# Kernel optimization log

Measured on AMD Instinct MI355X. Metric: run time of the kernel, lower is better.

## Reference

```python
import jax, jax.numpy as jnp
import numpy as np
from jax import lax

B, TIN, N, M, O, LM, TDEC = 64, 128, 256, 1024, 512, 2048, 64
LN_EPS = 1e-5


def setup_inputs() -> dict:
    key = jax.random.key(0)
    ks = jax.random.split(key, 32)
    s = 0.02
    p = lambda k, shape: (jax.random.normal(k, shape, jnp.float32) * s)
    z = lambda n: jnp.zeros((n,), jnp.float32)
    return {
        "X": jax.random.normal(ks[0], (B, TIN, N), jnp.float32),
        "Y0": jax.random.uniform(ks[1], (B, 1, O), jnp.float32),
        # encoder GRU, 2 layers (PyTorch layout: W_ih [3m,in], W_hh [3m,m])
        "enc_Wih0": p(ks[2], (3 * M, N)), "enc_Whh0": p(ks[3], (3 * M, M)),
        "enc_bih0": z(3 * M), "enc_bhh0": z(3 * M),
        "enc_Wih1": p(ks[4], (3 * M, M)), "enc_Whh1": p(ks[5], (3 * M, M)),
        "enc_bih1": z(3 * M), "enc_bhh1": z(3 * M),
        # decoder GRU, 2 layers (layer0 input dim = O)
        "dec_Wih0": p(ks[6], (3 * M, O)), "dec_Whh0": p(ks[7], (3 * M, M)),
        "dec_bih0": z(3 * M), "dec_bhh0": z(3 * M),
        "dec_Wih1": p(ks[8], (3 * M, M)), "dec_Whh1": p(ks[9], (3 * M, M)),
        "dec_bih1": z(3 * M), "dec_bhh1": z(3 * M),
        # decoder head
        "fc1_w": p(ks[10], (LM, M)), "fc1_b": z(LM),
        "ln_g": jnp.ones((LM,), jnp.float32), "ln_b": z(LM),
        "fc2_w": p(ks[11], (O, LM)), "fc2_b": z(O),
    }


def _gru_step(h, x, Wih, Whh, bih, bhh):
    # PyTorch GRU cell: gates ordered (r, z, n)
    gi = x @ Wih.T + bih          # [B, 3m]
    gh = h @ Whh.T + bhh          # [B, 3m]
    i_r, i_z, i_n = jnp.split(gi, 3, axis=-1)
    h_r, h_z, h_n = jnp.split(gh, 3, axis=-1)
    r = jax.nn.sigmoid(i_r + h_r)
    zg = jax.nn.sigmoid(i_z + h_z)
    n = jnp.tanh(i_n + r * h_n)
    return (1.0 - zg) * n + zg * h


def reference(X, Y0,
              enc_Wih0, enc_Whh0, enc_bih0, enc_bhh0,
              enc_Wih1, enc_Whh1, enc_bih1, enc_bhh1,
              dec_Wih0, dec_Whh0, dec_bih0, dec_bhh0,
              dec_Wih1, dec_Whh1, dec_bih1, dec_bhh1,
              fc1_w, fc1_b, ln_g, ln_b, fc2_w, fc2_b):
    batch = X.shape[0]
    # ---- encoder: 2-layer GRU over time ----
    seq = jnp.swapaxes(X, 0, 1)  # [T, B, n]
    enc_layers = [(enc_Wih0, enc_Whh0, enc_bih0, enc_bhh0),
                  (enc_Wih1, enc_Whh1, enc_bih1, enc_bhh1)]
    h_final = []
    for (Wih, Whh, bih, bhh) in enc_layers:
        def f(h, x, Wih=Wih, Whh=Whh, bih=bih, bhh=bhh):
            hn = _gru_step(h, x, Wih, Whh, bih, bhh)
            return hn, hn
        hT, seq = lax.scan(f, jnp.zeros((batch, M), X.dtype), seq)
        h_final.append(hT)

    dec0 = (dec_Wih0, dec_Whh0, dec_bih0, dec_bhh0)
    dec1 = (dec_Wih1, dec_Whh1, dec_bih1, dec_bhh1)
    y_init = Y0[:, 0, :]  # [B, o]

    def step(carry, _):
        h0, h1, y = carry
        h0n = _gru_step(h0, y, *dec0)
        h1n = _gru_step(h1, h0n, *dec1)
        z = h1n @ fc1_w.T + fc1_b                      # [B, l_m]
        mu = jnp.mean(z, axis=-1, keepdims=True)
        var = jnp.var(z, axis=-1, keepdims=True)
        z = (z - mu) * lax.rsqrt(var + LN_EPS) * ln_g + ln_b
        z = jax.nn.gelu(z, approximate=False)
        out = z @ fc2_w.T + fc2_b                      # [B, o]
        yn = jax.nn.softmax(out, axis=-1)
        return (h0n, h1n, yn), out

    _, outs = lax.scan(step, (h_final[0], h_final[1], y_init), None, length=TDEC)
    return jnp.swapaxes(outs, 0, 1)  # [B, TDEC, o]
```

## Files before the change

kernel.cpp:

```cpp
#include <hip/hip_runtime.h>
#include <math.h>

#define B 64
#define TIN 128
#define N_IN 256
#define M 1024
#define O_DIM 512
#define LM 2048
#define TDEC 64
#define M3 3072
#define CH 8

typedef short bf16x8 __attribute__((ext_vector_type(8)));
typedef float floatx4 __attribute__((ext_vector_type(4)));

__device__ __forceinline__ unsigned short f2bf(float f) {
    unsigned int u = __float_as_uint(f);
    u += 0x7FFFu + ((u >> 16) & 1u);
    return (unsigned short)(u >> 16);
}
__device__ __forceinline__ float sigm(float x) { return 1.f / (1.f + expf(-x)); }

__global__ __launch_bounds__(256) void cast_bf(const float* __restrict__ in,
                                               short* __restrict__ out, int n) {
    int i = blockIdx.x * 256 + threadIdx.x;
    if (i < n) out[i] = (short)f2bf(in[i]);
}

__global__ __launch_bounds__(256) void transpose_X_bf(const float* __restrict__ X,
                                                      short* __restrict__ Xt) {
    int idx = blockIdx.x * 256 + threadIdx.x;
    int n = idx & (N_IN - 1);
    int b = (idx >> 8) & (B - 1);
    int t = idx >> 14;
    Xt[idx] = (short)f2bf(X[(b * TIN + t) * N_IN + n]);
}

__global__ __launch_bounds__(256) void mfma_gemm_bias(
    const short* __restrict__ A, int lda,
    const short* __restrict__ W, int ldw,
    const float* __restrict__ bias,
    float* __restrict__ C, int ldc, int K) {
    int wave = threadIdx.x >> 6;
    int lane = threadIdx.x & 63;
    int r0 = blockIdx.y * 64 + wave * 16;
    int c0 = blockIdx.x * 16;
    int lrow = lane & 15;
    int ko8 = (lane >> 4) * 8;
    const short* ap = A + (size_t)(r0 + lrow) * lda + ko8;
    const short* wp = W + (size_t)(c0 + lrow) * ldw + ko8;
    floatx4 acc = {0.f, 0.f, 0.f, 0.f};
    #pragma unroll 4
    for (int k = 0; k < K; k += 32) {
        bf16x8 a = *(const bf16x8*)(ap + k);
        bf16x8 b = *(const bf16x8*)(wp + k);
        acc = __builtin_amdgcn_mfma_f32_16x16x32_bf16(a, b, acc, 0, 0, 0);
    }
    int col = c0 + lrow;
    float bv = bias[col];
    int rbase = r0 + (lane >> 4) * 4;
    #pragma unroll
    for (int i = 0; i < 4; i++)
        C[(size_t)(rbase + i) * ldc + col] = acc[i] + bv;
}

__global__ __launch_bounds__(256) void mfma_gemm_bias_ks(
    const short* __restrict__ A, int lda,
    const short* __restrict__ W, int ldw,
    const float* __restrict__ bias,
    float* __restrict__ C, int ldc, int K) {
    __shared__ float lds[4][64][4];
    int wave = threadIdx.x >> 6;
    int lane = threadIdx.x & 63;
    int r0 = blockIdx.y * 16;
    int c0 = blockIdx.x * 16;
    int Kq = K >> 2;
    int lrow = lane & 15;
    int ko8 = (lane >> 4) * 8;
    const short* ap = A + (size_t)(r0 + lrow) * lda + wave * Kq + ko8;
    const short* wp = W + (size_t)(c0 + lrow) * ldw + wave * Kq + ko8;
    floatx4 acc = {0.f, 0.f, 0.f, 0.f};
    #pragma unroll 4
    for (int k = 0; k < Kq; k += 32) {
        bf16x8 a = *(const bf16x8*)(ap + k);
        bf16x8 b = *(const bf16x8*)(wp + k);
        acc = __builtin_amdgcn_mfma_f32_16x16x32_bf16(a, b, acc, 0, 0, 0);
    }
    #pragma unroll
    for (int i = 0; i < 4; i++) lds[wave][lane][i] = acc[i];
    __syncthreads();
    int row = threadIdx.x >> 4, col = threadIdx.x & 15;
    int sl = (row >> 2) * 16 + col, rg = row & 3;
    float s = lds[0][sl][rg] + lds[1][sl][rg] + lds[2][sl][rg] + lds[3][sl][rg];
    C[(size_t)(r0 + row) * ldc + (c0 + col)] = s + bias[c0 + col];
}

__global__ __launch_bounds__(256) void gru_step_enc(
    const short* __restrict__ h_in_bf, const short* __restrict__ Whh,
    const float* __restrict__ gi, const float* __restrict__ bhh,
    float* __restrict__ h_f, short* __restrict__ h_out_bf,
    short* __restrict__ seq_out_bf) {
    __shared__ float lr[4][64][4], lz[4][64][4], lnn[4][64][4];
    int wave = threadIdx.x >> 6;
    int lane = threadIdx.x & 63;
    int m0 = blockIdx.x * 16;
    int r0 = blockIdx.y * 16;
    int lrow = lane & 15;
    int ko8 = (lane >> 4) * 8;
    const int Kq = M >> 2;
    const short* ap = h_in_bf + (size_t)(r0 + lrow) * M + wave * Kq + ko8;
    const short* wr = Whh + (size_t)(m0 + lrow) * M + wave * Kq + ko8;
    const short* wz = wr + (size_t)M * M;
    const short* wn = wr + (size_t)2 * M * M;
    floatx4 ar = {0.f, 0.f, 0.f, 0.f};
    floatx4 az = {0.f, 0.f, 0.f, 0.f};
    floatx4 ahn = {0.f, 0.f, 0.f, 0.f};
    #pragma unroll
    for (int k = 0; k < Kq; k += 32) {
        bf16x8 a = *(const bf16x8*)(ap + k);
        ar  = __builtin_amdgcn_mfma_f32_16x16x32_bf16(a, *(const bf16x8*)(wr + k), ar, 0, 0, 0);
        az  = __builtin_amdgcn_mfma_f32_16x16x32_bf16(a, *(const bf16x8*)(wz + k), az, 0, 0, 0);
        ahn = __builtin_amdgcn_mfma_f32_16x16x32_bf16(a, *(const bf16x8*)(wn + k), ahn, 0, 0, 0);
    }
    #pragma unroll
    for (int i = 0; i < 4; i++) {
        lr[wave][lane][i] = ar[i];
        lz[wave][lane][i] = az[i];
        lnn[wave][lane][i] = ahn[i];
    }
    __syncthreads();
    int row = threadIdx.x >> 4, col = threadIdx.x & 15;
    int sl = (row >> 2) * 16 + col, rg = row & 3;
    float sr = lr[0][sl][rg] + lr[1][sl][rg] + lr[2][sl][rg] + lr[3][sl][rg];
    float sz = lz[0][sl][rg] + lz[1][sl][rg] + lz[2][sl][rg] + lz[3][sl][rg];
    float sn = lnn[0][sl][rg] + lnn[1][sl][rg] + lnn[2][sl][rg] + lnn[3][sl][rg];
    int b = r0 + row, m = m0 + col;
    const float* gir = gi + (size_t)b * M3;
    float r = sigm(gir[m] + sr + bhh[m]);
    float z = sigm(gir[M + m] + sz + bhh[M + m]);
    float n = tanhf(gir[2 * M + m] + r * (sn + bhh[2 * M + m]));
    size_t hi = (size_t)b * M + m;
    float hv = (1.f - z) * n + z * h_f[hi];
    h_f[hi] = hv;
    short hb = (short)f2bf(hv);
    h_out_bf[hi] = hb;
    if (seq_out_bf) seq_out_bf[hi] = hb;
}

__global__ __launch_bounds__(256) void gru_step_dec(
    const short* __restrict__ x_bf, int Kx,
    const short* __restrict__ Wih,
    const short* __restrict__ h_in_bf, const short* __restrict__ Whh,
    const float* __restrict__ bih, const float* __restrict__ bhh,
    float* __restrict__ h_f, short* __restrict__ h_out_bf) {
    __shared__ float lr[4][64][4], lz[4][64][4], li[4][64][4], lh[4][64][4];
    int wave = threadIdx.x >> 6;
    int lane = threadIdx.x & 63;
    int m0 = blockIdx.x * 16;
    int r0 = blockIdx.y * 16;
    int lrow = lane & 15;
    int ko8 = (lane >> 4) * 8;
    floatx4 ar = {0.f, 0.f, 0.f, 0.f};
    floatx4 az = {0.f, 0.f, 0.f, 0.f};
    floatx4 ain = {0.f, 0.f, 0.f, 0.f};
    floatx4 ahn = {0.f, 0.f, 0.f, 0.f};
    {
        int Kq = Kx >> 2;
        const short* ap = x_bf + (size_t)(r0 + lrow) * Kx + wave * Kq + ko8;
        const short* wr = Wih + (size_t)(m0 + lrow) * Kx + wave * Kq + ko8;
        const short* wz = wr + (size_t)M * Kx;
        const short* wn = wr + (size_t)2 * M * Kx;
        #pragma unroll
        for (int k = 0; k < Kq; k += 32) {
            bf16x8 a = *(const bf16x8*)(ap + k);
            ar  = __builtin_amdgcn_mfma_f32_16x16x32_bf16(a, *(const bf16x8*)(wr + k), ar, 0, 0, 0);
            az  = __builtin_amdgcn_mfma_f32_16x16x32_bf16(a, *(const bf16x8*)(wz + k), az, 0, 0, 0);
            ain = __builtin_amdgcn_mfma_f32_16x16x32_bf16(a, *(const bf16x8*)(wn + k), ain, 0, 0, 0);
        }
    }
    {
        const int Kq = M >> 2;
        const short* ap = h_in_bf + (size_t)(r0 + lrow) * M + wave * Kq + ko8;
        const short* wr = Whh + (size_t)(m0 + lrow) * M + wave * Kq + ko8;
        const short* wz = wr + (size_t)M * M;
        const short* wn = wr + (size_t)2 * M * M;
        #pragma unroll
        for (int k = 0; k < Kq; k += 32) {
            bf16x8 a = *(const bf16x8*)(ap + k);
            ar  = __builtin_amdgcn_mfma_f32_16x16x32_bf16(a, *(const bf16x8*)(wr + k), ar, 0, 0, 0);
            az  = __builtin_amdgcn_mfma_f32_16x16x32_bf16(a, *(const bf16x8*)(wz + k), az, 0, 0, 0);
            ahn = __builtin_amdgcn_mfma_f32_16x16x32_bf16(a, *(const bf16x8*)(wn + k), ahn, 0, 0, 0);
        }
    }
    #pragma unroll
    for (int i = 0; i < 4; i++) {
        lr[wave][lane][i] = ar[i];
        lz[wave][lane][i] = az[i];
        li[wave][lane][i] = ain[i];
        lh[wave][lane][i] = ahn[i];
    }
    __syncthreads();
    int row = threadIdx.x >> 4, col = threadIdx.x & 15;
    int sl = (row >> 2) * 16 + col, rg = row & 3;
    float sr = lr[0][sl][rg] + lr[1][sl][rg] + lr[2][sl][rg] + lr[3][sl][rg];
    float sz = lz[0][sl][rg] + lz[1][sl][rg] + lz[2][sl][rg] + lz[3][sl][rg];
    float si = li[0][sl][rg] + li[1][sl][rg] + li[2][sl][rg] + li[3][sl][rg];
    float sh = lh[0][sl][rg] + lh[1][sl][rg] + lh[2][sl][rg] + lh[3][sl][rg];
    int b = r0 + row, m = m0 + col;
    float r = sigm(sr + bih[m] + bhh[m]);
    float z = sigm(sz + bih[M + m] + bhh[M + m]);
    float n = tanhf(si + bih[2 * M + m] + r * (sh + bhh[2 * M + m]));
    size_t hi = (size_t)b * M + m;
    float hv = (1.f - z) * n + z * h_f[hi];
    h_f[hi] = hv;
    h_out_bf[hi] = (short)f2bf(hv);
}

__global__ __launch_bounds__(256) void ln_gelu(const float* __restrict__ z,
                                               const float* __restrict__ g,
                                               const float* __restrict__ bt,
                                               short* __restrict__ zo) {
    __shared__ float red1[4], red2[4];
    int b = blockIdx.x, t = threadIdx.x;
    const float* row = z + (size_t)b * LM;
    float s = 0.f, ss = 0.f;
    for (int i = t; i < LM; i += 256) { float v = row[i]; s += v; ss += v * v; }
    #pragma unroll
    for (int off = 32; off > 0; off >>= 1) {
        s += __shfl_down(s, off, 64);
        ss += __shfl_down(ss, off, 64);
    }
    if ((t & 63) == 0) { red1[t >> 6] = s; red2[t >> 6] = ss; }
    __syncthreads();
    float S = red1[0] + red1[1] + red1[2] + red1[3];
    float SS = red2[0] + red2[1] + red2[2] + red2[3];
    float mu = S * (1.f / LM);
    float var = SS * (1.f / LM) - mu * mu;
    float inv = rsqrtf(var + 1e-5f);
    for (int i = t; i < LM; i += 256) {
        float v = (row[i] - mu) * inv * g[i] + bt[i];
        float gv = 0.5f * v * (1.f + erff(v * 0.70710678118654752f));
        zo[(size_t)b * LM + i] = (short)f2bf(gv);
    }
}

__global__ __launch_bounds__(256) void softmax_row(const float* __restrict__ logits,
                                                   int ldl, short* __restrict__ y) {
    __shared__ float redm[4], reds[4];
    int b = blockIdx.x, t = threadIdx.x;
    const float* row = logits + (size_t)b * ldl;
    float v0 = row[t], v1 = row[t + 256];
    float mx = fmaxf(v0, v1);
    #pragma unroll
    for (int off = 32; off > 0; off >>= 1) mx = fmaxf(mx, __shfl_down(mx, off, 64));
    if ((t & 63) == 0) redm[t >> 6] = mx;
    __syncthreads();
    mx = fmaxf(fmaxf(redm[0], redm[1]), fmaxf(redm[2], redm[3]));
    float e0 = expf(v0 - mx), e1 = expf(v1 - mx);
    float s = e0 + e1;
    #pragma unroll
    for (int off = 32; off > 0; off >>= 1) s += __shfl_down(s, off, 64);
    if ((t & 63) == 0) reds[t >> 6] = s;
    __syncthreads();
    s = reds[0] + reds[1] + reds[2] + reds[3];
    float inv = 1.f / s;
    y[b * O_DIM + t] = (short)f2bf(e0 * inv);
    y[b * O_DIM + t + 256] = (short)f2bf(e1 * inv);
}

extern "C" void kernel_launch(void* const* d_in, const int* in_sizes, int n_in,
                              void* d_out, int out_size, void* d_ws, size_t ws_size,
                              hipStream_t stream) {
    const float* X        = (const float*)d_in[0];
    const float* Y0       = (const float*)d_in[1];
    const float* enc_Wih0 = (const float*)d_in[2];
    const float* enc_Whh0 = (const float*)d_in[3];
    const float* enc_bih0 = (const float*)d_in[4];
    const float* enc_bhh0 = (const float*)d_in[5];
    const float* enc_Wih1 = (const float*)d_in[6];
    const float* enc_Whh1 = (const float*)d_in[7];
    const float* enc_bih1 = (const float*)d_in[8];
    const float* enc_bhh1 = (const float*)d_in[9];
    const float* dec_Wih0 = (const float*)d_in[10];
    const float* dec_Whh0 = (const float*)d_in[11];
    const float* dec_bih0 = (const float*)d_in[12];
    const float* dec_bhh0 = (const float*)d_in[13];
    const float* dec_Wih1 = (const float*)d_in[14];
    const float* dec_Whh1 = (const float*)d_in[15];
    const float* dec_bih1 = (const float*)d_in[16];
    const float* dec_bhh1 = (const float*)d_in[17];
    const float* fc1_w    = (const float*)d_in[18];
    const float* fc1_b    = (const float*)d_in[19];
    const float* ln_g     = (const float*)d_in[20];
    const float* ln_b     = (const float*)d_in[21];
    const float* fc2_w    = (const float*)d_in[22];
    const float* fc2_b    = (const float*)d_in[23];
    float* out = (float*)d_out;

    char* p = (char*)d_ws;
    auto carve = [&](size_t bytes) {
        void* r = p;
        p += (bytes + 255) & ~(size_t)255;
        return r;
    };
    short* Xt    = (short*)carve((size_t)TIN * B * N_IN * 2);
    short* seqA  = (short*)carve((size_t)TIN * B * M * 2);
    float* gi_ch = (float*)carve((size_t)CH * B * M3 * 4);
    short* we_ih0 = (short*)carve((size_t)M3 * N_IN * 2);
    short* we_hh0 = (short*)carve((size_t)M3 * M * 2);
    short* we_ih1 = (short*)carve((size_t)M3 * M * 2);
    short* we_hh1 = (short*)carve((size_t)M3 * M * 2);
    short* wd_ih0 = (short*)carve((size_t)M3 * O_DIM * 2);
    short* wd_hh0 = (short*)carve((size_t)M3 * M * 2);
    short* wd_ih1 = (short*)carve((size_t)M3 * M * 2);
    short* wd_hh1 = (short*)carve((size_t)M3 * M * 2);
    short* wfc1   = (short*)carve((size_t)LM * M * 2);
    short* wfc2   = (short*)carve((size_t)O_DIM * LM * 2);
    float* h0f = (float*)carve((size_t)B * M * 4);
    float* h1f = (float*)carve((size_t)B * M * 4);
    short* h0b = (short*)carve((size_t)2 * B * M * 2);
    short* h1b = (short*)carve((size_t)2 * B * M * 2);
    short* yb  = (short*)carve((size_t)B * O_DIM * 2);
    float* zb  = (float*)carve((size_t)B * LM * 4);
    short* zbb = (short*)carve((size_t)B * LM * 2);

    auto cast = [&](const float* src, short* dst, int n) {
        cast_bf<<<(n + 255) / 256, 256, 0, stream>>>(src, dst, n);
    };
    cast(enc_Wih0, we_ih0, M3 * N_IN);
    cast(enc_Whh0, we_hh0, M3 * M);
    cast(enc_Wih1, we_ih1, M3 * M);
    cast(enc_Whh1, we_hh1, M3 * M);
    cast(dec_Wih0, wd_ih0, M3 * O_DIM);
    cast(dec_Whh0, wd_hh0, M3 * M);
    cast(dec_Wih1, wd_ih1, M3 * M);
    cast(dec_Whh1, wd_hh1, M3 * M);
    cast(fc1_w, wfc1, LM * M);
    cast(fc2_w, wfc2, O_DIM * LM);
    cast(Y0, yb, B * O_DIM);
    transpose_X_bf<<<(TIN * B * N_IN) / 256, 256, 0, stream>>>(X, Xt);

    hipMemsetAsync(h0f, 0, (size_t)B * M * 4, stream);
    hipMemsetAsync(h1f, 0, (size_t)B * M * 4, stream);
    hipMemsetAsync(h0b, 0, (size_t)B * M * 2, stream);
    hipMemsetAsync(h1b, 0, (size_t)B * M * 2, stream);

    dim3 gruGrid(M / 16, B / 16);

    for (int layer = 0; layer < 2; layer++) {
        const short* Wih = layer ? we_ih1 : we_ih0;
        const short* Whh = layer ? we_hh1 : we_hh0;
        const float* bih = layer ? enc_bih1 : enc_bih0;
        const float* bhh = layer ? enc_bhh1 : enc_bhh0;
        const short* inseq = layer ? seqA : Xt;
        const int Kin = layer ? M : N_IN;
        float* hf = layer ? h1f : h0f;
        short* hb = layer ? h1b : h0b;
        for (int c = 0; c < TIN / CH; c++) {
            mfma_gemm_bias<<<dim3(M3 / 16, CH * B / 64), 256, 0, stream>>>(
                inseq + (size_t)c * CH * B * Kin, Kin, Wih, Kin, bih,
                gi_ch, M3, Kin);
            for (int tt = 0; tt < CH; tt++) {
                int t = c * CH + tt;
                int pin = t & 1, pout = pin ^ 1;
                short* so = (layer == 0) ? (seqA + (size_t)t * B * M) : nullptr;
                gru_step_enc<<<gruGrid, 256, 0, stream>>>(
                    hb + (size_t)pin * B * M, Whh,
                    gi_ch + (size_t)tt * B * M3, bhh,
                    hf, hb + (size_t)pout * B * M, so);
            }
        }
    }

    for (int t = 0; t < TDEC; t++) {
        int pin = t & 1, pout = pin ^ 1;
        gru_step_dec<<<gruGrid, 256, 0, stream>>>(
            yb, O_DIM, wd_ih0,
            h0b + (size_t)pin * B * M, wd_hh0,
            dec_bih0, dec_bhh0, h0f, h0b + (size_t)pout * B * M);
        gru_step_dec<<<gruGrid, 256, 0, stream>>>(
            h0b + (size_t)pout * B * M, M, wd_ih1,
            h1b + (size_t)pin * B * M, wd_hh1,
            dec_bih1, dec_bhh1, h1f, h1b + (size_t)pout * B * M);
        mfma_gemm_bias_ks<<<dim3(LM / 16, B / 16), 256, 0, stream>>>(
            h1b + (size_t)pout * B * M, M, wfc1, M, fc1_b, zb, LM, M);
        ln_gelu<<<B, 256, 0, stream>>>(zb, ln_g, ln_b, zbb);
        mfma_gemm_bias_ks<<<dim3(O_DIM / 16, B / 16), 256, 0, stream>>>(
            zbb, LM, wfc2, LM, fc2_b, out + (size_t)t * O_DIM, TDEC * O_DIM, LM);
        softmax_row<<<B, 256, 0, stream>>>(out + (size_t)t * O_DIM,
                                           TDEC * O_DIM, yb);
    }
}
```

Before: 5.534 ms.

## Wavefront-fuse encoder GRU layers and fold softmax and LayerNorm into neighbouring GEMMs

```diff
diff --git a/kernel.cpp b/kernel.cpp
--- a/kernel.cpp
+++ b/kernel.cpp
@@ -64,11 +64,260 @@
         C[(size_t)(rbase + i) * ldc + col] = acc[i] + bv;
 }
 
-__global__ __launch_bounds__(256) void mfma_gemm_bias_ks(
+__device__ __forceinline__ void gru_dec_core(
+    const short* x_bf, int Kx,
+    const short* Wih,
+    const short* h_in_bf, const short* Whh,
+    const float* bih, const float* bhh,
+    float* h_f, short* h_out_bf,
+    float (*lr)[64][4], float (*lz)[64][4],
+    float (*li)[64][4], float (*lh)[64][4]) {
+    int wave = threadIdx.x >> 6;
+    int lane = threadIdx.x & 63;
+    int m0 = blockIdx.x * 16;
+    int r0 = blockIdx.y * 16;
+    int lrow = lane & 15;
+    int ko8 = (lane >> 4) * 8;
+    floatx4 ar = {0.f, 0.f, 0.f, 0.f};
+    floatx4 az = {0.f, 0.f, 0.f, 0.f};
+    floatx4 ain = {0.f, 0.f, 0.f, 0.f};
+    floatx4 ahn = {0.f, 0.f, 0.f, 0.f};
+    {
+        int Kq = Kx >> 2;
+        const short* ap = x_bf + (size_t)(r0 + lrow) * Kx + wave * Kq + ko8;
+        const short* wr = Wih + (size_t)(m0 + lrow) * Kx + wave * Kq + ko8;
+        const short* wz = wr + (size_t)M * Kx;
+        const short* wn = wr + (size_t)2 * M * Kx;
+        #pragma unroll
+        for (int k = 0; k < Kq; k += 32) {
+            bf16x8 a = *(const bf16x8*)(ap + k);
+            ar  = __builtin_amdgcn_mfma_f32_16x16x32_bf16(a, *(const bf16x8*)(wr + k), ar, 0, 0, 0);
+            az  = __builtin_amdgcn_mfma_f32_16x16x32_bf16(a, *(const bf16x8*)(wz + k), az, 0, 0, 0);
+            ain = __builtin_amdgcn_mfma_f32_16x16x32_bf16(a, *(const bf16x8*)(wn + k), ain, 0, 0, 0);
+        }
+    }
+    {
+        const int Kq = M >> 2;
+        const short* ap = h_in_bf + (size_t)(r0 + lrow) * M + wave * Kq + ko8;
+        const short* wr = Whh + (size_t)(m0 + lrow) * M + wave * Kq + ko8;
+        const short* wz = wr + (size_t)M * M;
+        const short* wn = wr + (size_t)2 * M * M;
+        #pragma unroll
+        for (int k = 0; k < Kq; k += 32) {
+            bf16x8 a = *(const bf16x8*)(ap + k);
+            ar  = __builtin_amdgcn_mfma_f32_16x16x32_bf16(a, *(const bf16x8*)(wr + k), ar, 0, 0, 0);
+            az  = __builtin_amdgcn_mfma_f32_16x16x32_bf16(a, *(const bf16x8*)(wz + k), az, 0, 0, 0);
+            ahn = __builtin_amdgcn_mfma_f32_16x16x32_bf16(a, *(const bf16x8*)(wn + k), ahn, 0, 0, 0);
+        }
+    }
+    #pragma unroll
+    for (int i = 0; i < 4; i++) {
+        lr[wave][lane][i] = ar[i];
+        lz[wave][lane][i] = az[i];
+        li[wave][lane][i] = ain[i];
+        lh[wave][lane][i] = ahn[i];
+    }
+    __syncthreads();
+    int row = threadIdx.x >> 4, col = threadIdx.x & 15;
+    int sl = (row >> 2) * 16 + col, rg = row & 3;
+    float sr = lr[0][sl][rg] + lr[1][sl][rg] + lr[2][sl][rg] + lr[3][sl][rg];
+    float sz = lz[0][sl][rg] + lz[1][sl][rg] + lz[2][sl][rg] + lz[3][sl][rg];
+    float si = li[0][sl][rg] + li[1][sl][rg] + li[2][sl][rg] + li[3][sl][rg];
+    float sh = lh[0][sl][rg] + lh[1][sl][rg] + lh[2][sl][rg] + lh[3][sl][rg];
+    int b = r0 + row, m = m0 + col;
+    float r = sigm(sr + bih[m] + bhh[m]);
+    float z = sigm(sz + bih[M + m] + bhh[M + m]);
+    float n = tanhf(si + bih[2 * M + m] + r * (sh + bhh[2 * M + m]));
+    size_t hi = (size_t)b * M + m;
+    float hv = (1.f - z) * n + z * h_f[hi];
+    h_f[hi] = hv;
+    h_out_bf[hi] = (short)f2bf(hv);
+}
+
+__global__ __launch_bounds__(256) void gru_step_dec(
+    const short* __restrict__ x_bf, int Kx,
+    const short* __restrict__ Wih,
+    const short* __restrict__ h_in_bf, const short* __restrict__ Whh,
+    const float* __restrict__ bih, const float* __restrict__ bhh,
+    float* __restrict__ h_f, short* __restrict__ h_out_bf) {
+    __shared__ float lds[4][4][64][4];
+    gru_dec_core(x_bf, Kx, Wih, h_in_bf, Whh, bih, bhh, h_f, h_out_bf,
+                 lds[0], lds[1], lds[2], lds[3]);
+}
+
+__global__ __launch_bounds__(256) void enc_step(
+    const short* __restrict__ h0_in, const short* __restrict__ Whh0,
+    const float* __restrict__ gi, const float* __restrict__ bhh0,
+    float* __restrict__ h0f, short* __restrict__ h0_out, short* __restrict__ seq_out,
+    const short* __restrict__ x1, const short* __restrict__ Wih1,
+    const short* __restrict__ h1_in, const short* __restrict__ Whh1,
+    const float* __restrict__ bih1, const float* __restrict__ bhh1,
+    float* __restrict__ h1f, short* __restrict__ h1_out) {
+    __shared__ float lds[4][4][64][4];
+    if (blockIdx.z == 1) {
+        if (!x1) return;
+        gru_dec_core(x1, M, Wih1, h1_in, Whh1, bih1, bhh1, h1f, h1_out,
+                     lds[0], lds[1], lds[2], lds[3]);
+        return;
+    }
+    if (!gi) return;
+    int wave = threadIdx.x >> 6;
+    int lane = threadIdx.x & 63;
+    int m0 = blockIdx.x * 16;
+    int r0 = blockIdx.y * 16;
+    int lrow = lane & 15;
+    int ko8 = (lane >> 4) * 8;
+    const int Kq = M >> 2;
+    const short* ap = h0_in + (size_t)(r0 + lrow) * M + wave * Kq + ko8;
+    const short* wr = Whh0 + (size_t)(m0 + lrow) * M + wave * Kq + ko8;
+    const short* wz = wr + (size_t)M * M;
+    const short* wn = wr + (size_t)2 * M * M;
+    floatx4 ar = {0.f, 0.f, 0.f, 0.f};
+    floatx4 az = {0.f, 0.f, 0.f, 0.f};
+    floatx4 ahn = {0.f, 0.f, 0.f, 0.f};
+    #pragma unroll
+    for (int k = 0; k < Kq; k += 32) {
+        bf16x8 a = *(const bf16x8*)(ap + k);
+        ar  = __builtin_amdgcn_mfma_f32_16x16x32_bf16(a, *(const bf16x8*)(wr + k), ar, 0, 0, 0);
+        az  = __builtin_amdgcn_mfma_f32_16x16x32_bf16(a, *(const bf16x8*)(wz + k), az, 0, 0, 0);
+        ahn = __builtin_amdgcn_mfma_f32_16x16x32_bf16(a, *(const bf16x8*)(wn + k), ahn, 0, 0, 0);
+    }
+    #pragma unroll
+    for (int i = 0; i < 4; i++) {
+        lds[0][wave][lane][i] = ar[i];
+        lds[1][wave][lane][i] = az[i];
+        lds[2][wave][lane][i] = ahn[i];
+    }
+    __syncthreads();
+    int row = threadIdx.x >> 4, col = threadIdx.x & 15;
+    int sl = (row >> 2) * 16 + col, rg = row & 3;
+    float sr = lds[0][0][sl][rg] + lds[0][1][sl][rg] + lds[0][2][sl][rg] + lds[0][3][sl][rg];
+    float sz = lds[1][0][sl][rg] + lds[1][1][sl][rg] + lds[1][2][sl][rg] + lds[1][3][sl][rg];
+    float sn = lds[2][0][sl][rg] + lds[2][1][sl][rg] + lds[2][2][sl][rg] + lds[2][3][sl][rg];
+    int b = r0 + row, m = m0 + col;
+    const float* gir = gi + (size_t)b * M3;
+    float r = sigm(gir[m] + sr + bhh0[m]);
+    float z = sigm(gir[M + m] + sz + bhh0[M + m]);
+    float n = tanhf(gir[2 * M + m] + r * (sn + bhh0[2 * M + m]));
+    size_t hi = (size_t)b * M + m;
+    float hv = (1.f - z) * n + z * h0f[hi];
+    h0f[hi] = hv;
+    short hb = (short)f2bf(hv);
+    h0_out[hi] = hb;
+    seq_out[hi] = hb;
+}
+
+__global__ __launch_bounds__(256) void gru0_sm(
+    const float* __restrict__ prev_logits, int ldl,
+    const short* __restrict__ y0_bf,
+    const short* __restrict__ Wih,
+    const short* __restrict__ h_in_bf, const short* __restrict__ Whh,
+    const float* __restrict__ bih, const float* __restrict__ bhh,
+    float* __restrict__ h_f, short* __restrict__ h_out_bf) {
+    __shared__ short xs[16 * O_DIM];
+    __shared__ float lds[4][4][64][4];
+    int wave = threadIdx.x >> 6;
+    int lane = threadIdx.x & 63;
+    int m0 = blockIdx.x * 16;
+    int r0 = blockIdx.y * 16;
+    int rr = wave * 4 + (lane >> 4);
+    int cl = lane & 15;
+    if (prev_logits) {
+        const float* rowp = prev_logits + (size_t)(r0 + rr) * ldl + cl * 32;
+        float v[32];
+        float mx = -3.4e38f;
+        #pragma unroll
+        for (int j = 0; j < 32; j++) { v[j] = rowp[j]; mx = fmaxf(mx, v[j]); }
+        #pragma unroll
+        for (int off = 1; off < 16; off <<= 1) mx = fmaxf(mx, __shfl_xor(mx, off, 16));
+        float s = 0.f;
+        #pragma unroll
+        for (int j = 0; j < 32; j++) { v[j] = __expf(v[j] - mx); s += v[j]; }
+        #pragma unroll
+        for (int off = 1; off < 16; off <<= 1) s += __shfl_xor(s, off, 16);
+        float inv = 1.f / s;
+        #pragma unroll
+        for (int j = 0; j < 32; j += 2) {
+            unsigned int pk = (unsigned int)f2bf(v[j] * inv)
+                            | ((unsigned int)f2bf(v[j + 1] * inv) << 16);
+            int byte = ((rr * O_DIM + cl * 32 + j) * 2) ^ ((rr & 7) << 4);
+            *(unsigned int*)((char*)xs + byte) = pk;
+        }
+    } else {
+        const short* rowp = y0_bf + (size_t)(r0 + rr) * O_DIM + cl * 32;
+        #pragma unroll
+        for (int j = 0; j < 32; j += 2) {
+            unsigned int pk = (unsigned int)(unsigned short)rowp[j]
+                            | ((unsigned int)(unsigned short)rowp[j + 1] << 16);
+            int byte = ((rr * O_DIM + cl * 32 + j) * 2) ^ ((rr & 7) << 4);
+            *(unsigned int*)((char*)xs + byte) = pk;
+        }
+    }
+    __syncthreads();
+    int lrow = lane & 15;
+    int ko8 = (lane >> 4) * 8;
+    floatx4 ar = {0.f, 0.f, 0.f, 0.f};
+    floatx4 az = {0.f, 0.f, 0.f, 0.f};
+    floatx4 ain = {0.f, 0.f, 0.f, 0.f};
+    floatx4 ahn = {0.f, 0.f, 0.f, 0.f};
+    {
+        const int Kq = O_DIM >> 2;
+        const short* wr = Wih + (size_t)(m0 + lrow) * O_DIM + wave * Kq + ko8;
+        const short* wz = wr + (size_t)M * O_DIM;
+        const short* wn = wr + (size_t)2 * M * O_DIM;
+        #pragma unroll
+        for (int k = 0; k < Kq; k += 32) {
+            int abyte = ((lrow * O_DIM + wave * Kq + ko8 + k) * 2) ^ ((lrow & 7) << 4);
+            bf16x8 a = *(const bf16x8*)((const char*)xs + abyte);
+            ar  = __builtin_amdgcn_mfma_f32_16x16x32_bf16(a, *(const bf16x8*)(wr + k), ar, 0, 0, 0);
+            az  = __builtin_amdgcn_mfma_f32_16x16x32_bf16(a, *(const bf16x8*)(wz + k), az, 0, 0, 0);
+            ain = __builtin_amdgcn_mfma_f32_16x16x32_bf16(a, *(const bf16x8*)(wn + k), ain, 0, 0, 0);
+        }
+    }
+    {
+        const int Kq = M >> 2;
+        const short* ap = h_in_bf + (size_t)(r0 + lrow) * M + wave * Kq + ko8;
+        const short* wr = Whh + (size_t)(m0 + lrow) * M + wave * Kq + ko8;
+        const short* wz = wr + (size_t)M * M;
+        const short* wn = wr + (size_t)2 * M * M;
+        #pragma unroll
+        for (int k = 0; k < Kq; k += 32) {
+            bf16x8 a = *(const bf16x8*)(ap + k);
+            ar  = __builtin_amdgcn_mfma_f32_16x16x32_bf16(a, *(const bf16x8*)(wr + k), ar, 0, 0, 0);
+            az  = __builtin_amdgcn_mfma_f32_16x16x32_bf16(a, *(const bf16x8*)(wz + k), az, 0, 0, 0);
+            ahn = __builtin_amdgcn_mfma_f32_16x16x32_bf16(a, *(const bf16x8*)(wn + k), ahn, 0, 0, 0);
+        }
+    }
+    #pragma unroll
+    for (int i = 0; i < 4; i++) {
+        lds[0][wave][lane][i] = ar[i];
+        lds[1][wave][lane][i] = az[i];
+        lds[2][wave][lane][i] = ain[i];
+        lds[3][wave][lane][i] = ahn[i];
+    }
+    __syncthreads();
+    int row = threadIdx.x >> 4, col = threadIdx.x & 15;
+    int sl = (row >> 2) * 16 + col, rg = row & 3;
+    float sr = lds[0][0][sl][rg] + lds[0][1][sl][rg] + lds[0][2][sl][rg] + lds[0][3][sl][rg];
+    float sz = lds[1][0][sl][rg] + lds[1][1][sl][rg] + lds[1][2][sl][rg] + lds[1][3][sl][rg];
+    float si = lds[2][0][sl][rg] + lds[2][1][sl][rg] + lds[2][2][sl][rg] + lds[2][3][sl][rg];
+    float sh = lds[3][0][sl][rg] + lds[3][1][sl][rg] + lds[3][2][sl][rg] + lds[3][3][sl][rg];
+    int b = r0 + row, m = m0 + col;
+    float r = sigm(sr + bih[m] + bhh[m]);
+    float z = sigm(sz + bih[M + m] + bhh[M + m]);
+    float n = tanhf(si + bih[2 * M + m] + r * (sh + bhh[2 * M + m]));
+    size_t hi = (size_t)b * M + m;
+    float hv = (1.f - z) * n + z * h_f[hi];
+    h_f[hi] = hv;
+    h_out_bf[hi] = (short)f2bf(hv);
+}
+
+__global__ __launch_bounds__(256) void fc1_stats(
     const short* __restrict__ A, int lda,
     const short* __restrict__ W, int ldw,
     const float* __restrict__ bias,
-    float* __restrict__ C, int ldc, int K) {
+    float* __restrict__ C, int ldc, int K,
+    float* __restrict__ stats) {
     __shared__ float lds[4][64][4];
     int wave = threadIdx.x >> 6;
     int lane = threadIdx.x & 63;
@@ -92,180 +341,62 @@
     int row = threadIdx.x >> 4, col = threadIdx.x & 15;
     int sl = (row >> 2) * 16 + col, rg = row & 3;
     float s = lds[0][sl][rg] + lds[1][sl][rg] + lds[2][sl][rg] + lds[3][sl][rg];
-    C[(size_t)(r0 + row) * ldc + (c0 + col)] = s + bias[c0 + col];
-}
-
-__global__ __launch_bounds__(256) void gru_step_enc(
-    const short* __restrict__ h_in_bf, const short* __restrict__ Whh,
-    const float* __restrict__ gi, const float* __restrict__ bhh,
-    float* __restrict__ h_f, short* __restrict__ h_out_bf,
-    short* __restrict__ seq_out_bf) {
-    __shared__ float lr[4][64][4], lz[4][64][4], lnn[4][64][4];
+    float val = s + bias[c0 + col];
+    C[(size_t)(r0 + row) * ldc + (c0 + col)] = val;
+    float sv = val, sq = val * val;
+    #pragma unroll
+    for (int off = 1; off < 16; off <<= 1) {
+        sv += __shfl_xor(sv, off, 16);
+        sq += __shfl_xor(sq, off, 16);
+    }
+    if ((threadIdx.x & 15) == 0) {
+        atomicAdd(&stats[r0 + row], sv);
+        atomicAdd(&stats[B + r0 + row], sq);
+    }
+}
+
+__global__ __launch_bounds__(256) void fc2_lngelu(
+    const float* __restrict__ zrow,
+    const short* __restrict__ W,
+    const float* __restrict__ bias,
+    const float* __restrict__ stats,
+    const float* __restrict__ g, const float* __restrict__ bt,
+    float* __restrict__ C, int ldc) {
+    __shared__ float lds[4][64][4];
     int wave = threadIdx.x >> 6;
     int lane = threadIdx.x & 63;
-    int m0 = blockIdx.x * 16;
     int r0 = blockIdx.y * 16;
+    int c0 = blockIdx.x * 16;
+    const int Kq = LM >> 2;
     int lrow = lane & 15;
     int ko8 = (lane >> 4) * 8;
-    const int Kq = M >> 2;
-    const short* ap = h_in_bf + (size_t)(r0 + lrow) * M + wave * Kq + ko8;
-    const short* wr = Whh + (size_t)(m0 + lrow) * M + wave * Kq + ko8;
-    const short* wz = wr + (size_t)M * M;
-    const short* wn = wr + (size_t)2 * M * M;
-    floatx4 ar = {0.f, 0.f, 0.f, 0.f};
-    floatx4 az = {0.f, 0.f, 0.f, 0.f};
-    floatx4 ahn = {0.f, 0.f, 0.f, 0.f};
-    #pragma unroll
+    int r = r0 + lrow;
+    float mu = stats[r] * (1.f / LM);
+    float var = stats[B + r] * (1.f / LM) - mu * mu;
+    float inv = rsqrtf(var + 1e-5f);
+    const float* zp = zrow + (size_t)r * LM + wave * Kq + ko8;
+    const float* gp = g + wave * Kq + ko8;
+    const float* bp = bt + wave * Kq + ko8;
+    const short* wp = W + (size_t)(c0 + lrow) * LM + wave * Kq + ko8;
+    floatx4 acc = {0.f, 0.f, 0.f, 0.f};
     for (int k = 0; k < Kq; k += 32) {
-        bf16x8 a = *(const bf16x8*)(ap + k);
-        ar  = __builtin_amdgcn_mfma_f32_16x16x32_bf16(a, *(const bf16x8*)(wr + k), ar, 0, 0, 0);
-        az  = __builtin_amdgcn_mfma_f32_16x16x32_bf16(a, *(const bf16x8*)(wz + k), az, 0, 0, 0);
-        ahn = __builtin_amdgcn_mfma_f32_16x16x32_bf16(a, *(const bf16x8*)(wn + k), ahn, 0, 0, 0);
-    }
-    #pragma unroll
-    for (int i = 0; i < 4; i++) {
-        lr[wave][lane][i] = ar[i];
-        lz[wave][lane][i] = az[i];
-        lnn[wave][lane][i] = ahn[i];
-    }
+        bf16x8 a;
+        #pragma unroll
+        for (int j = 0; j < 8; j++) {
+            float zn = (zp[k + j] - mu) * inv * gp[k + j] + bp[k + j];
+            float ge = 0.5f * zn * (1.f + erff(zn * 0.70710678118654752f));
+            a[j] = (short)f2bf(ge);
+        }
+        bf16x8 b = *(const bf16x8*)(wp + k);
+        acc = __builtin_amdgcn_mfma_f32_16x16x32_bf16(a, b, acc, 0, 0, 0);
+    }
+    #pragma unroll
+    for (int i = 0; i < 4; i++) lds[wave][lane][i] = acc[i];
     __syncthreads();
     int row = threadIdx.x >> 4, col = threadIdx.x & 15;
     int sl = (row >> 2) * 16 + col, rg = row & 3;
-    float sr = lr[0][sl][rg] + lr[1][sl][rg] + lr[2][sl][rg] + lr[3][sl][rg];
-    float sz = lz[0][sl][rg] + lz[1][sl][rg] + lz[2][sl][rg] + lz[3][sl][rg];
-    float sn = lnn[0][sl][rg] + lnn[1][sl][rg] + lnn[2][sl][rg] + lnn[3][sl][rg];
-    int b = r0 + row, m = m0 + col;
-    const float* gir = gi + (size_t)b * M3;
-    float r = sigm(gir[m] + sr + bhh[m]);
-    float z = sigm(gir[M + m] + sz + bhh[M + m]);
-    float n = tanhf(gir[2 * M + m] + r * (sn + bhh[2 * M + m]));
-    size_t hi = (size_t)b * M + m;
-    float hv = (1.f - z) * n + z * h_f[hi];
-    h_f[hi] = hv;
-    short hb = (short)f2bf(hv);
-    h_out_bf[hi] = hb;
-    if (seq_out_bf) seq_out_bf[hi] = hb;
-}
-
-__global__ __launch_bounds__(256) void gru_step_dec(
-    const short* __restrict__ x_bf, int Kx,
-    const short* __restrict__ Wih,
-    const short* __restrict__ h_in_bf, const short* __restrict__ Whh,
-    const float* __restrict__ bih, const float* __restrict__ bhh,
-    float* __restrict__ h_f, short* __restrict__ h_out_bf) {
-    __shared__ float lr[4][64][4], lz[4][64][4], li[4][64][4], lh[4][64][4];
-    int wave = threadIdx.x >> 6;
-    int lane = threadIdx.x & 63;
-    int m0 = blockIdx.x * 16;
-    int r0 = blockIdx.y * 16;
-    int lrow = lane & 15;
-    int ko8 = (lane >> 4) * 8;
-    floatx4 ar = {0.f, 0.f, 0.f, 0.f};
-    floatx4 az = {0.f, 0.f, 0.f, 0.f};
-    floatx4 ain = {0.f, 0.f, 0.f, 0.f};
-    floatx4 ahn = {0.f, 0.f, 0.f, 0.f};
-    {
-        int Kq = Kx >> 2;
-        const short* ap = x_bf + (size_t)(r0 + lrow) * Kx + wave * Kq + ko8;
-        const short* wr = Wih + (size_t)(m0 + lrow) * Kx + wave * Kq + ko8;
-        const short* wz = wr + (size_t)M * Kx;
-        const short* wn = wr + (size_t)2 * M * Kx;
-        #pragma unroll
-        for (int k = 0; k < Kq; k += 32) {
-            bf16x8 a = *(const bf16x8*)(ap + k);
-            ar  = __builtin_amdgcn_mfma_f32_16x16x32_bf16(a, *(const bf16x8*)(wr + k), ar, 0, 0, 0);
-            az  = __builtin_amdgcn_mfma_f32_16x16x32_bf16(a, *(const bf16x8*)(wz + k), az, 0, 0, 0);
-            ain = __builtin_amdgcn_mfma_f32_16x16x32_bf16(a, *(const bf16x8*)(wn + k), ain, 0, 0, 0);
-        }
-    }
-    {
-        const int Kq = M >> 2;
-        const short* ap = h_in_bf + (size_t)(r0 + lrow) * M + wave * Kq + ko8;
-        const short* wr = Whh + (size_t)(m0 + lrow) * M + wave * Kq + ko8;
-        const short* wz = wr + (size_t)M * M;
-        const short* wn = wr + (size_t)2 * M * M;
-        #pragma unroll
-        for (int k = 0; k < Kq; k += 32) {
-            bf16x8 a = *(const bf16x8*)(ap + k);
-            ar  = __builtin_amdgcn_mfma_f32_16x16x32_bf16(a, *(const bf16x8*)(wr + k), ar, 0, 0, 0);
-            az  = __builtin_amdgcn_mfma_f32_16x16x32_bf16(a, *(const bf16x8*)(wz + k), az, 0, 0, 0);
-            ahn = __builtin_amdgcn_mfma_f32_16x16x32_bf16(a, *(const bf16x8*)(wn + k), ahn, 0, 0, 0);
-        }
-    }
-    #pragma unroll
-    for (int i = 0; i < 4; i++) {
-        lr[wave][lane][i] = ar[i];
-        lz[wave][lane][i] = az[i];
-        li[wave][lane][i] = ain[i];
-        lh[wave][lane][i] = ahn[i];
-    }
-    __syncthreads();
-    int row = threadIdx.x >> 4, col = threadIdx.x & 15;
-    int sl = (row >> 2) * 16 + col, rg = row & 3;
-    float sr = lr[0][sl][rg] + lr[1][sl][rg] + lr[2][sl][rg] + lr[3][sl][rg];
-    float sz = lz[0][sl][rg] + lz[1][sl][rg] + lz[2][sl][rg] + lz[3][sl][rg];
-    float si = li[0][sl][rg] + li[1][sl][rg] + li[2][sl][rg] + li[3][sl][rg];
-    float sh = lh[0][sl][rg] + lh[1][sl][rg] + lh[2][sl][rg] + lh[3][sl][rg];
-    int b = r0 + row, m = m0 + col;
-    float r = sigm(sr + bih[m] + bhh[m]);
-    float z = sigm(sz + bih[M + m] + bhh[M + m]);
-    float n = tanhf(si + bih[2 * M + m] + r * (sh + bhh[2 * M + m]));
-    size_t hi = (size_t)b * M + m;
-    float hv = (1.f - z) * n + z * h_f[hi];
-    h_f[hi] = hv;
-    h_out_bf[hi] = (short)f2bf(hv);
-}
-
-__global__ __launch_bounds__(256) void ln_gelu(const float* __restrict__ z,
-                                               const float* __restrict__ g,
-                                               const float* __restrict__ bt,
-                                               short* __restrict__ zo) {
-    __shared__ float red1[4], red2[4];
-    int b = blockIdx.x, t = threadIdx.x;
-    const float* row = z + (size_t)b * LM;
-    float s = 0.f, ss = 0.f;
-    for (int i = t; i < LM; i += 256) { float v = row[i]; s += v; ss += v * v; }
-    #pragma unroll
-    for (int off = 32; off > 0; off >>= 1) {
-        s += __shfl_down(s, off, 64);
-        ss += __shfl_down(ss, off, 64);
-    }
-    if ((t & 63) == 0) { red1[t >> 6] = s; red2[t >> 6] = ss; }
-    __syncthreads();
-    float S = red1[0] + red1[1] + red1[2] + red1[3];
-    float SS = red2[0] + red2[1] + red2[2] + red2[3];
-    float mu = S * (1.f / LM);
-    float var = SS * (1.f / LM) - mu * mu;
-    float inv = rsqrtf(var + 1e-5f);
-    for (int i = t; i < LM; i += 256) {
-        float v = (row[i] - mu) * inv * g[i] + bt[i];
-        float gv = 0.5f * v * (1.f + erff(v * 0.70710678118654752f));
-        zo[(size_t)b * LM + i] = (short)f2bf(gv);
-    }
-}
-
-__global__ __launch_bounds__(256) void softmax_row(const float* __restrict__ logits,
-                                                   int ldl, short* __restrict__ y) {
-    __shared__ float redm[4], reds[4];
-    int b = blockIdx.x, t = threadIdx.x;
-    const float* row = logits + (size_t)b * ldl;
-    float v0 = row[t], v1 = row[t + 256];
-    float mx = fmaxf(v0, v1);
-    #pragma unroll
-    for (int off = 32; off > 0; off >>= 1) mx = fmaxf(mx, __shfl_down(mx, off, 64));
-    if ((t & 63) == 0) redm[t >> 6] = mx;
-    __syncthreads();
-    mx = fmaxf(fmaxf(redm[0], redm[1]), fmaxf(redm[2], redm[3]));
-    float e0 = expf(v0 - mx), e1 = expf(v1 - mx);
-    float s = e0 + e1;
-    #pragma unroll
-    for (int off = 32; off > 0; off >>= 1) s += __shfl_down(s, off, 64);
-    if ((t & 63) == 0) reds[t >> 6] = s;
-    __syncthreads();
-    s = reds[0] + reds[1] + reds[2] + reds[3];
-    float inv = 1.f / s;
-    y[b * O_DIM + t] = (short)f2bf(e0 * inv);
-    y[b * O_DIM + t + 256] = (short)f2bf(e1 * inv);
+    float s = lds[0][sl][rg] + lds[1][sl][rg] + lds[2][sl][rg] + lds[3][sl][rg];
+    C[(size_t)(r0 + row) * ldc + (c0 + col)] = s + bias[c0 + col];
 }
 
 extern "C" void kernel_launch(void* const* d_in, const int* in_sizes, int n_in,
@@ -322,7 +453,7 @@
     short* h1b = (short*)carve((size_t)2 * B * M * 2);
     short* yb  = (short*)carve((size_t)B * O_DIM * 2);
     float* zb  = (float*)carve((size_t)B * LM * 4);
-    short* zbb = (short*)carve((size_t)B * LM * 2);
+    float* lnstats = (float*)carve((size_t)TDEC * 2 * B * 4);
 
     auto cast = [&](const float* src, short* dst, int n) {
         cast_bf<<<(n + 255) / 256, 256, 0, stream>>>(src, dst, n);
@@ -344,50 +475,44 @@
     hipMemsetAsync(h1f, 0, (size_t)B * M * 4, stream);
     hipMemsetAsync(h0b, 0, (size_t)B * M * 2, stream);
     hipMemsetAsync(h1b, 0, (size_t)B * M * 2, stream);
+    hipMemsetAsync(lnstats, 0, (size_t)TDEC * 2 * B * 4, stream);
+
+    for (int t = 0; t <= TIN; t++) {
+        if (t < TIN && (t % CH) == 0) {
+            int c = t / CH;
+            mfma_gemm_bias<<<dim3(M3 / 16, CH * B / 64), 256, 0, stream>>>(
+                Xt + (size_t)c * CH * B * N_IN, N_IN, we_ih0, N_IN, enc_bih0,
+                gi_ch, M3, N_IN);
+        }
+        const float* gi_t = (t < TIN) ? gi_ch + (size_t)(t % CH) * B * M3 : nullptr;
+        const short* x1 = (t >= 1) ? seqA + (size_t)(t - 1) * B * M : nullptr;
+        int p0 = t & 1;
+        int p1 = (t - 1) & 1;
+        enc_step<<<dim3(M / 16, B / 16, 2), 256, 0, stream>>>(
+            h0b + (size_t)p0 * B * M, we_hh0, gi_t, enc_bhh0,
+            h0f, h0b + (size_t)(p0 ^ 1) * B * M,
+            seqA + (size_t)(t < TIN ? t : 0) * B * M,
+            x1, we_ih1, h1b + (size_t)(p1 & 1) * B * M, we_hh1,
+            enc_bih1, enc_bhh1, h1f, h1b + (size_t)((p1 & 1) ^ 1) * B * M);
+    }
 
     dim3 gruGrid(M / 16, B / 16);
-
-    for (int layer = 0; layer < 2; layer++) {
-        const short* Wih = layer ? we_ih1 : we_ih0;
-        const short* Whh = layer ? we_hh1 : we_hh0;
-        const float* bih = layer ? enc_bih1 : enc_bih0;
-        const float* bhh = layer ? enc_bhh1 : enc_bhh0;
-        const short* inseq = layer ? seqA : Xt;
-        const int Kin = layer ? M : N_IN;
-        float* hf = layer ? h1f : h0f;
-        short* hb = layer ? h1b : h0b;
-        for (int c = 0; c < TIN / CH; c++) {
-            mfma_gemm_bias<<<dim3(M3 / 16, CH * B / 64), 256, 0, stream>>>(
-                inseq + (size_t)c * CH * B * Kin, Kin, Wih, Kin, bih,
-                gi_ch, M3, Kin);
-            for (int tt = 0; tt < CH; tt++) {
-                int t = c * CH + tt;
-                int pin = t & 1, pout = pin ^ 1;
-                short* so = (layer == 0) ? (seqA + (size_t)t * B * M) : nullptr;
-                gru_step_enc<<<gruGrid, 256, 0, stream>>>(
-                    hb + (size_t)pin * B * M, Whh,
-                    gi_ch + (size_t)tt * B * M3, bhh,
-                    hf, hb + (size_t)pout * B * M, so);
-            }
-        }
-    }
-
     for (int t = 0; t < TDEC; t++) {
         int pin = t & 1, pout = pin ^ 1;
-        gru_step_dec<<<gruGrid, 256, 0, stream>>>(
-            yb, O_DIM, wd_ih0,
+        const float* plog = t ? out + (size_t)(t - 1) * O_DIM : nullptr;
+        gru0_sm<<<gruGrid, 256, 0, stream>>>(
+            plog, TDEC * O_DIM, yb, wd_ih0,
             h0b + (size_t)pin * B * M, wd_hh0,
             dec_bih0, dec_bhh0, h0f, h0b + (size_t)pout * B * M);
         gru_step_dec<<<gruGrid, 256, 0, stream>>>(
             h0b + (size_t)pout * B * M, M, wd_ih1,
             h1b + (size_t)pin * B * M, wd_hh1,
             dec_bih1, dec_bhh1, h1f, h1b + (size_t)pout * B * M);
-        mfma_gemm_bias_ks<<<dim3(LM / 16, B / 16), 256, 0, stream>>>(
-            h1b + (size_t)pout * B * M, M, wfc1, M, fc1_b, zb, LM, M);
-        ln_gelu<<<B, 256, 0, stream>>>(zb, ln_g, ln_b, zbb);
-        mfma_gemm_bias_ks<<<dim3(O_DIM / 16, B / 16), 256, 0, stream>>>(
-            zbb, LM, wfc2, LM, fc2_b, out + (size_t)t * O_DIM, TDEC * O_DIM, LM);
-        softmax_row<<<B, 256, 0, stream>>>(out + (size_t)t * O_DIM,
-                                           TDEC * O_DIM, yb);
-    }
-}
+        fc1_stats<<<dim3(LM / 16, B / 16), 256, 0, stream>>>(
+            h1b + (size_t)pout * B * M, M, wfc1, M, fc1_b, zb, LM, M,
+            lnstats + (size_t)t * 2 * B);
+        fc2_lngelu<<<dim3(O_DIM / 16, B / 16), 256, 0, stream>>>(
+            zb, wfc2, fc2_b, lnstats + (size_t)t * 2 * B, ln_g, ln_b,
+            out + (size_t)t * O_DIM, TDEC * O_DIM);
+    }
+}
```

Measured after the change: 6.358 ms. 14.9% more time.
